# Kernel tuning notes

Hardware: AMD Instinct MI355X
Metric: run time of the kernel (lower is better)

Reference implementation:

```python
import jax, jax.numpy as jnp
import numpy as np

B, C, HD, H, W = 4, 64, 64, 64, 64  # batch, input_dim, hidden_dim, spatial


def conv1x1(x, w, b):
    # x: [B, Cin, H, W], w: [Cout, Cin], b: [Cout]
    return jnp.einsum('oc,bchw->bohw', w, x) + b[None, :, None, None]


def setup_inputs() -> dict:
    key = jax.random.key(0)
    ks = jax.random.split(key, 16)
    sc = lambda cin: 1.0 / np.sqrt(cin)
    d = {
        'h': jax.random.normal(ks[0], (B, C, H, W), jnp.float32),
        'm': jax.random.normal(ks[1], (B, C, H, W), jnp.float32),
        'Wq': jax.random.normal(ks[2], (HD, C), jnp.float32) * sc(C),
        'bq': jnp.zeros((HD,), jnp.float32),
        'Wk': jax.random.normal(ks[3], (HD, C), jnp.float32) * sc(C),
        'bk': jnp.zeros((HD,), jnp.float32),
        'Wk2': jax.random.normal(ks[4], (HD, C), jnp.float32) * sc(C),
        'bk2': jnp.zeros((HD,), jnp.float32),
        'Wv': jax.random.normal(ks[5], (C, C), jnp.float32) * sc(C),
        'bv': jnp.zeros((C,), jnp.float32),
        'Wv2': jax.random.normal(ks[6], (C, C), jnp.float32) * sc(C),
        'bv2': jnp.zeros((C,), jnp.float32),
        'Wz': jax.random.normal(ks[7], (2 * C, 2 * C), jnp.float32) * sc(2 * C),
        'bz': jnp.zeros((2 * C,), jnp.float32),
        'Wm': jax.random.normal(ks[8], (3 * C, 3 * C), jnp.float32) * sc(3 * C),
        'bm': jnp.zeros((3 * C,), jnp.float32),
    }
    return d


def reference(h, m, Wq, bq, Wk, bk, Wk2, bk2, Wv, bv, Wv2, bv2, Wz, bz, Wm, bm):
    b, c, hh, ww = h.shape
    n = hh * ww
    K_h = conv1x1(h, Wk, bk).reshape(b, HD, n)            # [B, HD, N]
    Q_h = conv1x1(h, Wq, bq).reshape(b, HD, n).transpose(0, 2, 1)  # [B, N, HD]
    V_h = conv1x1(h, Wv, bv).reshape(b, c, n)             # [B, C, N]
    K_m = conv1x1(m, Wk2, bk2).reshape(b, HD, n)
    V_m = conv1x1(m, Wv2, bv2).reshape(b, c, n)

    A_h = jax.nn.softmax(jnp.einsum('bnd,bdk->bnk', Q_h, K_h), axis=-1)  # [B, N, N]
    Z_h = jnp.einsum('bnk,bck->bcn', A_h, V_h).reshape(b, c, hh, ww)
    A_m = jax.nn.softmax(jnp.einsum('bnd,bdk->bnk', Q_h, K_m), axis=-1)
    Z_m = jnp.einsum('bnk,bck->bcn', A_m, V_m).reshape(b, c, hh, ww)

    Z = conv1x1(jnp.concatenate([Z_h, Z_m], axis=1), Wz, bz)   # [B, 2C, H, W]
    combined = conv1x1(jnp.concatenate([Z, h], axis=1), Wm, bm)  # [B, 3C, H, W]
    mo, mg, mi = jnp.split(combined, 3, axis=1)
    mi = jax.nn.sigmoid(mi)
    new_m = (1.0 - mi) * m + mi * jnp.tanh(mg)
    new_h = jax.nn.sigmoid(mo) * new_m
    return (new_h, new_m)
```

## Files before the change

### kernel.cpp

```cpp
#include <hip/hip_runtime.h>

#define BN 4
#define NN 4096
#define SPLITK 2
#define LOG2E 1.44269504f
#define MFIX 36.0f

typedef __attribute__((ext_vector_type(8))) __bf16 bf16x8;
typedef __attribute__((ext_vector_type(4))) short s16x4;
typedef __attribute__((ext_vector_type(4))) float f32x4;
typedef unsigned short u16;

__device__ __forceinline__ u16 f2bf(float x) {
  unsigned int u = __builtin_bit_cast(unsigned int, x);
  u = (u + 0x7fffu + ((u >> 16) & 1u)) >> 16;
  return (u16)u;
}
__device__ __forceinline__ u16 f2bfs(float x) {
  __bf16 b = (__bf16)x;
  return __builtin_bit_cast(u16, b);
}
__device__ __forceinline__ float bf2f(u16 s) {
  unsigned int u = ((unsigned int)s) << 16;
  return __builtin_bit_cast(float, u);
}

__device__ __forceinline__ f32x4 mfma16(s16x4 a, s16x4 b, f32x4 c) {
#if defined(__HIP_DEVICE_COMPILE__)
  return __builtin_amdgcn_mfma_f32_16x16x16bf16_1k(a, b, c, 0, 0, 0);
#else
  return c;
#endif
}

__device__ __forceinline__ void gld16(const u16* g, u16* l) {
#if defined(__HIP_DEVICE_COMPILE__)
  __builtin_amdgcn_global_load_lds(
      (const __attribute__((address_space(1))) void*)g,
      (__attribute__((address_space(3))) void*)l, 16, 0, 0);
#else
  (void)g; (void)l;
#endif
}

#define PACK16(A, P0, P1)                                                          \
    P0.x = (unsigned)f2bf(A[0]) | ((unsigned)f2bf(A[1]) << 16);                    \
    P0.y = (unsigned)f2bf(A[2]) | ((unsigned)f2bf(A[3]) << 16);                    \
    P0.z = (unsigned)f2bf(A[4]) | ((unsigned)f2bf(A[5]) << 16);                    \
    P0.w = (unsigned)f2bf(A[6]) | ((unsigned)f2bf(A[7]) << 16);                    \
    P1.x = (unsigned)f2bf(A[8]) | ((unsigned)f2bf(A[9]) << 16);                    \
    P1.y = (unsigned)f2bf(A[10]) | ((unsigned)f2bf(A[11]) << 16);                  \
    P1.z = (unsigned)f2bf(A[12]) | ((unsigned)f2bf(A[13]) << 16);                  \
    P1.w = (unsigned)f2bf(A[14]) | ((unsigned)f2bf(A[15]) << 16);

__global__ void fuse_w_kernel(const float* __restrict__ Wz, const float* __restrict__ bz,
                              const float* __restrict__ Wm, const float* __restrict__ bm,
                              u16* __restrict__ Wbig, float* __restrict__ bbig) {
  int idx = blockIdx.x * 256 + threadIdx.x;
  if (idx < 192 * 192) {
    int o = idx / 192, c = idx - o * 192;
    float v;
    if (c < 128) {
      float s = 0.f;
      for (int j = 0; j < 128; ++j) s = fmaf(Wm[o * 192 + j], Wz[j * 128 + c], s);
      v = s;
    } else {
      v = Wm[o * 192 + c];
    }
    Wbig[idx] = f2bf(v);
  }
  if (idx < 192) {
    float s = bm[idx];
    for (int j = 0; j < 128; ++j) s = fmaf(Wm[idx * 192 + j], bz[j], s);
    bbig[idx] = s;
  }
}

__global__ __launch_bounds__(256) void proj2_kernel(
    const float* __restrict__ h, const float* __restrict__ m,
    const float* __restrict__ Wq, const float* __restrict__ bq,
    const float* __restrict__ Wk, const float* __restrict__ bk,
    const float* __restrict__ Wk2, const float* __restrict__ bk2,
    const float* __restrict__ Wv, const float* __restrict__ bv,
    const float* __restrict__ Wv2, const float* __restrict__ bv2,
    u16* __restrict__ Q, u16* __restrict__ Kh, u16* __restrict__ Km,
    u16* __restrict__ Vh, u16* __restrict__ Vm, u16* __restrict__ hT) {
  __shared__ float xs[64][65];
  int blk = blockIdx.x;
  int ntile = blk & 63, b = (blk >> 6) & 3, pid = blk >> 8;
  int n0 = ntile * 64;
  int t = threadIdx.x, nl = t & 63;
  const float* src = (pid == 2 || pid == 4) ? m : h;
  {
    int c0 = (t >> 6) * 16;
#pragma unroll
    for (int i = 0; i < 16; ++i) {
      int c = c0 + i;
      xs[c][nl] = src[((size_t)(b * 64) + c) * NN + n0 + nl];
    }
  }
  __syncthreads();
  int w = __builtin_amdgcn_readfirstlane(t >> 6);
  size_t nrow = (size_t)b * NN + n0 + nl;
  float acc[16];
  if (pid == 5) {
#pragma unroll
    for (int i = 0; i < 16; ++i) acc[i] = xs[w * 16 + i][nl];
  } else {
    const float* W = pid == 0 ? Wq : pid == 1 ? Wk : pid == 2 ? Wk2 : pid == 3 ? Wv : Wv2;
    const float* bs = pid == 0 ? bq : pid == 1 ? bk : pid == 2 ? bk2 : pid == 3 ? bv : bv2;
#pragma unroll
    for (int i = 0; i < 16; ++i) acc[i] = bs[w * 16 + i];
    for (int c = 0; c < 64; ++c) {
      float x = xs[c][nl];
#pragma unroll
      for (int i = 0; i < 16; ++i) acc[i] = fmaf(W[(w * 16 + i) * 64 + c], x, acc[i]);
    }
    if (pid == 0) {
#pragma unroll
      for (int i = 0; i < 16; ++i) acc[i] *= LOG2E;
    }
  }
  if (pid == 3 || pid == 4) {
    u16* dst = (pid == 3) ? Vh : Vm;
#pragma unroll
    for (int i = 0; i < 16; ++i) {
      int o = w * 16 + i;
      dst[((size_t)(b * 64) + o) * NN + n0 + nl] = f2bf(acc[i]);
    }
  } else {
    u16* dst = pid == 0 ? Q : pid == 1 ? Kh : pid == 2 ? Km : hT;
    uint4 p0, p1;
    PACK16(acc, p0, p1);
    uint4* dp = (uint4*)(dst + nrow * 64 + w * 16);
    dp[0] = p0; dp[1] = p1;
  }
}

__global__ __launch_bounds__(256) void flash6_kernel(
    const u16* __restrict__ Qg, const u16* __restrict__ Khg,
    const u16* __restrict__ Kmg, const u16* __restrict__ Vhg,
    const u16* __restrict__ Vmg, u16* __restrict__ Opart,
    float* __restrict__ Lpart) {
  __shared__ u16 Kl[2][4096];
  __shared__ u16 Vl[2][4096];
  int blk = blockIdx.x;
  int qt = blk & 63, attn = (blk >> 6) & 1, b = (blk >> 7) & 3, split = blk >> 9;
  const u16* K = (attn ? Kmg : Khg) + (size_t)b * NN * 64;
  const u16* V = (attn ? Vmg : Vhg) + (size_t)b * 64 * NN;
  int t = threadIdx.x, wave = t >> 6, lane = t & 63, col = lane & 15, quad = lane >> 4;
  int row0 = qt * 64 + wave * 16;

  const u16* qp = Qg + (size_t)b * NN * 64 + (size_t)(row0 + col) * 64 + quad * 8;
  bf16x8 bq0 = *(const bf16x8*)(const void*)qp;
  bf16x8 bq1 = *(const bf16x8*)(const void*)(qp + 32);

  f32x4 O[4];
#pragma unroll
  for (int i = 0; i < 4; ++i) O[i] = f32x4{0.f, 0.f, 0.f, 0.f};
  f32x4 lacc = {0.f, 0.f, 0.f, 0.f};
  int sp8 = split * 8 + b * 2 + attn;

  const int kbase = split * (NN / SPLITK);
  const int TILES = NN / SPLITK / 64;

#define STAGE(BUF, K0)                                                           \
  _Pragma("unroll") for (int jj = 0; jj < 2; ++jj) {                             \
    int p = jj * 256 + t;                                 \
    int row_ = p >> 3;                                                           \
    int jc_ = (p & 7) ^ (row_ & 7);          \
    gld16(K + (size_t)((K0) + row_) * 64 + jc_ * 8, &Kl[BUF][p * 8]);            \
    gld16(V + (size_t)row_ * NN + (K0) + jc_ * 8, &Vl[BUF][p * 8]);              \
  }

  STAGE(0, kbase);

  for (int kt = 0; kt < TILES; ++kt) {
    __syncthreads();
    int cur = kt & 1;
    if (kt + 1 < TILES) { STAGE(cur ^ 1, kbase + (kt + 1) * 64); }
    const u16* Kb = &Kl[cur][0];
    const u16* Vb = &Vl[cur][0];
    f32x4 St[4];
#pragma unroll
    for (int nt = 0; nt < 4; ++nt) {
      int row = nt * 16 + col;
      int ph0 = row * 8 + (quad ^ (col & 7));
      int ph1 = row * 8 + ((4 + quad) ^ (col & 7));
      bf16x8 a0 = *(const bf16x8*)(const void*)(Kb + ph0 * 8);
      bf16x8 a1 = *(const bf16x8*)(const void*)(Kb + ph1 * 8);
      f32x4 acc = {0.f, 0.f, 0.f, 0.f};
      acc = __builtin_amdgcn_mfma_f32_16x16x32_bf16(a0, bq0, acc, 0, 0, 0);
      acc = __builtin_amdgcn_mfma_f32_16x16x32_bf16(a1, bq1, acc, 0, 0, 0);
      St[nt] = acc;
    }
    s16x4 pfrag[4];
#pragma unroll
    for (int nt = 0; nt < 4; ++nt) {
      f32x4 p;
#pragma unroll
      for (int r = 0; r < 4; ++r) p[r] = __builtin_exp2f(St[nt][r] - MFIX);
      lacc += p;
      s16x4 pf;
#pragma unroll
      for (int r = 0; r < 4; ++r) pf[r] = (short)f2bfs(p[r]);
      pfrag[nt] = pf;
    }
#pragma unroll
    for (int nt = 0; nt < 4; ++nt) {
      int j = nt * 2 + (quad >> 1);
#pragma unroll
      for (int ct = 0; ct < 4; ++ct) {
        int c = ct * 16 + col;
        int ph = c * 8 + (j ^ (col & 7));
        s16x4 vf = *(const s16x4*)(const void*)(Vb + ph * 8 + (quad & 1) * 4);
        O[ct] = mfma16(pfrag[nt], vf, O[ct]);
      }
    }
  }
#undef STAGE

#pragma unroll
  for (int ct = 0; ct < 4; ++ct)
#pragma unroll
    for (int r = 0; r < 4; ++r) {
      size_t q = (size_t)row0 + quad * 4 + r;
      Opart[((size_t)sp8 * NN + q) * 64 + ct * 16 + col] = f2bfs(O[ct][r]);
    }
  float lsum = (lacc[0] + lacc[1]) + (lacc[2] + lacc[3]);
  lsum += __shfl_xor(lsum, 16);
  lsum += __shfl_xor(lsum, 32);
  if (lane < 16) Lpart[(size_t)sp8 * NN + row0 + lane] = lsum;
}

__global__ __launch_bounds__(256) void merge_kernel(
    const u16* __restrict__ Opart, const float* __restrict__ Lpart,
    u16* __restrict__ Zh, u16* __restrict__ Zm) {
  int g = blockIdx.x * 256 + threadIdx.x;
  int c = g & 63;
  int q = (g >> 6) & (NN - 1);
  int b2 = g >> 18;
  size_t i0 = (size_t)b2 * NN + q;
  size_t i1 = (size_t)(8 + b2) * NN + q;
  float L = Lpart[i0] + Lpart[i1];
  float o = bf2f(Opart[i0 * 64 + c]) + bf2f(Opart[i1 * 64 + c]);
  float z = o / L;
  u16* Z = (b2 & 1) ? Zm : Zh;
  int b = b2 >> 1;
  Z[((size_t)b * NN + q) * 64 + c] = f2bfs(z);
}

__global__ __launch_bounds__(256) void epi2_kernel(
    const u16* __restrict__ Wb, const float* __restrict__ bb,
    const u16* __restrict__ Zh, const u16* __restrict__ Zm,
    const u16* __restrict__ hT, const float* __restrict__ mglob,
    float* __restrict__ out) {
  int blk = blockIdx.x;
  int ng = blk * 16;
  int b = ng >> 12;
  int t = threadIdx.x, wave = t >> 6, lane = t & 63, col = lane & 15, quad = lane >> 4;
  size_t nrow = ((size_t)ng + col) * 64;
  bf16x8 bfr[6];
  bfr[0] = *(const bf16x8*)(const void*)(Zh + nrow + quad * 8);
  bfr[1] = *(const bf16x8*)(const void*)(Zh + nrow + 32 + quad * 8);
  bfr[2] = *(const bf16x8*)(const void*)(Zm + nrow + quad * 8);
  bfr[3] = *(const bf16x8*)(const void*)(Zm + nrow + 32 + quad * 8);
  bfr[4] = *(const bf16x8*)(const void*)(hT + nrow + quad * 8);
  bfr[5] = *(const bf16x8*)(const void*)(hT + nrow + 32 + quad * 8);
  f32x4 acc[3];
#pragma unroll
  for (int j = 0; j < 3; ++j) {
    int mt = wave + j * 4;
#pragma unroll
    for (int r = 0; r < 4; ++r) acc[j][r] = bb[mt * 16 + quad * 4 + r];
  }
#pragma unroll
  for (int ks = 0; ks < 6; ++ks) {
#pragma unroll
    for (int j = 0; j < 3; ++j) {
      int mt = wave + j * 4;
      bf16x8 af = *(const bf16x8*)(const void*)(Wb + (size_t)(mt * 16 + col) * 192 + ks * 32 + quad * 8);
      acc[j] = __builtin_amdgcn_mfma_f32_16x16x32_bf16(af, bfr[ks], acc[j], 0, 0, 0);
    }
  }
  int nloc = (ng & (NN - 1)) + col;
#pragma unroll
  for (int r = 0; r < 4; ++r) {
    int o = wave * 16 + quad * 4 + r;
    float mo = acc[0][r], mgt = acc[1][r], mi = acc[2][r];
    float si = 1.f / (1.f + __builtin_exp2f(-mi * LOG2E));
    float tg = 1.f - 2.f / (__builtin_exp2f(2.f * LOG2E * mgt) + 1.f);
    float mv = mglob[(size_t)(b * 64 + o) * NN + nloc];
    float nm = (1.f - si) * mv + si * tg;
    float nh = nm / (1.f + __builtin_exp2f(-mo * LOG2E));
    out[(size_t)(b * 64 + o) * NN + nloc] = nh;
    out[(size_t)BN * 64 * NN + (size_t)(b * 64 + o) * NN + nloc] = nm;
  }
}

extern "C" void kernel_launch(void* const* d_in, const int* in_sizes, int n_in,
                              void* d_out, int out_size, void* d_ws, size_t ws_size,
                              hipStream_t stream) {
  const float* h = (const float*)d_in[0];
  const float* m = (const float*)d_in[1];
  const float* Wq = (const float*)d_in[2];
  const float* bq = (const float*)d_in[3];
  const float* Wk = (const float*)d_in[4];
  const float* bk = (const float*)d_in[5];
  const float* Wk2 = (const float*)d_in[6];
  const float* bk2 = (const float*)d_in[7];
  const float* Wv = (const float*)d_in[8];
  const float* bv = (const float*)d_in[9];
  const float* Wv2 = (const float*)d_in[10];
  const float* bv2 = (const float*)d_in[11];
  const float* Wz = (const float*)d_in[12];
  const float* bz = (const float*)d_in[13];
  const float* Wm = (const float*)d_in[14];
  const float* bm = (const float*)d_in[15];
  float* out = (float*)d_out;

  size_t off = 0;
  auto alloc = [&](size_t bytes) {
    void* p = (char*)d_ws + off;
    off += (bytes + 255) & ~(size_t)255;
    return p;
  };
  const size_t bn64 = (size_t)BN * NN * 64;
  u16* Q  = (u16*)alloc(bn64 * 2);
  u16* Kh = (u16*)alloc(bn64 * 2);
  u16* Km = (u16*)alloc(bn64 * 2);
  u16* Vh = (u16*)alloc(bn64 * 2);
  u16* Vm = (u16*)alloc(bn64 * 2);
  u16* hT = (u16*)alloc(bn64 * 2);
  u16* Zh = (u16*)alloc(bn64 * 2);
  u16* Zm = (u16*)alloc(bn64 * 2);
  u16* Opart = (u16*)alloc((size_t)SPLITK * 8 * NN * 64 * 2);
  float* Lpart = (float*)alloc((size_t)SPLITK * 8 * NN * 4);
  u16* Wbigbf = (u16*)alloc(192 * 192 * 2);
  float* bbig = (float*)alloc(192 * 4);
  (void)ws_size; (void)in_sizes; (void)n_in; (void)out_size;

  fuse_w_kernel<<<144, 256, 0, stream>>>(Wz, bz, Wm, bm, Wbigbf, bbig);
  proj2_kernel<<<6 * BN * 64, 256, 0, stream>>>(h, m, Wq, bq, Wk, bk, Wk2, bk2, Wv, bv,
                                                Wv2, bv2, Q, Kh, Km, Vh, Vm, hT);
  flash6_kernel<<<SPLITK * BN * 2 * 64, 256, 0, stream>>>(Q, Kh, Km, Vh, Vm, Opart, Lpart);
  merge_kernel<<<(BN * 2 * NN * 64) / 256, 256, 0, stream>>>(Opart, Lpart, Zh, Zm);
  epi2_kernel<<<(BN * NN) / 16, 256, 0, stream>>>(Wbigbf, bbig, Zh, Zm, hT, m, out);
}
```

Measured before the change: 206.6 us.

## Fuse split-K merge into epilogue, widen flash blocks to 512 threads

Removes the separate merge kernel. The epilogue now reads both split-K partial outputs and their row sums, normalises them and feeds the result straight into the MFMA projection, which drops the Zh/Zm round trip through global memory. The flash attention kernel moves to 512-thread blocks covering 128 query rows, with a block order that interleaves batch, attention and split, so each staged K/V tile serves twice as many queries. The weight-fusion kernel is rewritten to use one block per output row with the Wm row held in shared memory. The trade-off is fewer, larger attention blocks, which may lower occupancy and latency hiding.

```diff
diff --git a/kernel.cpp b/kernel.cpp
--- a/kernel.cpp
+++ b/kernel.cpp
@@ -53,26 +53,27 @@
     P1.z = (unsigned)f2bf(A[12]) | ((unsigned)f2bf(A[13]) << 16);                  \
     P1.w = (unsigned)f2bf(A[14]) | ((unsigned)f2bf(A[15]) << 16);
 
-__global__ void fuse_w_kernel(const float* __restrict__ Wz, const float* __restrict__ bz,
-                              const float* __restrict__ Wm, const float* __restrict__ bm,
-                              u16* __restrict__ Wbig, float* __restrict__ bbig) {
-  int idx = blockIdx.x * 256 + threadIdx.x;
-  if (idx < 192 * 192) {
-    int o = idx / 192, c = idx - o * 192;
-    float v;
-    if (c < 128) {
-      float s = 0.f;
-      for (int j = 0; j < 128; ++j) s = fmaf(Wm[o * 192 + j], Wz[j * 128 + c], s);
-      v = s;
-    } else {
-      v = Wm[o * 192 + c];
-    }
-    Wbig[idx] = f2bf(v);
-  }
-  if (idx < 192) {
-    float s = bm[idx];
-    for (int j = 0; j < 128; ++j) s = fmaf(Wm[idx * 192 + j], bz[j], s);
-    bbig[idx] = s;
+__global__ __launch_bounds__(256) void fuse_w2_kernel(
+    const float* __restrict__ Wz, const float* __restrict__ bz,
+    const float* __restrict__ Wm, const float* __restrict__ bm,
+    u16* __restrict__ Wbig, float* __restrict__ bbig) {
+  __shared__ float wrow[128];
+  __shared__ float bzs[128];
+  int o = blockIdx.x;
+  int t = threadIdx.x;
+  if (t < 128) { wrow[t] = Wm[o * 192 + t]; bzs[t] = bz[t]; }
+  __syncthreads();
+  if (t < 128) {
+    float s = 0.f;
+#pragma unroll 4
+    for (int j = 0; j < 128; ++j) s = fmaf(wrow[j], Wz[j * 128 + t], s);
+    Wbig[o * 192 + t] = f2bf(s);
+  } else if (t < 192) {
+    Wbig[o * 192 + t] = f2bf(Wm[o * 192 + t]);
+  } else if (t == 192) {
+    float s = bm[o];
+    for (int j = 0; j < 128; ++j) s = fmaf(wrow[j], bzs[j], s);
+    bbig[o] = s;
   }
 }
 
@@ -137,7 +138,7 @@
   }
 }
 
-__global__ __launch_bounds__(256) void flash6_kernel(
+__global__ __launch_bounds__(512) void flash7_kernel(
     const u16* __restrict__ Qg, const u16* __restrict__ Khg,
     const u16* __restrict__ Kmg, const u16* __restrict__ Vhg,
     const u16* __restrict__ Vmg, u16* __restrict__ Opart,
@@ -145,11 +146,12 @@
   __shared__ u16 Kl[2][4096];
   __shared__ u16 Vl[2][4096];
   int blk = blockIdx.x;
-  int qt = blk & 63, attn = (blk >> 6) & 1, b = (blk >> 7) & 3, split = blk >> 9;
+  int combo = blk & 15, qt = blk >> 4;
+  int attn = combo & 1, b = (combo >> 1) & 3, split = combo >> 3;
   const u16* K = (attn ? Kmg : Khg) + (size_t)b * NN * 64;
   const u16* V = (attn ? Vmg : Vhg) + (size_t)b * 64 * NN;
   int t = threadIdx.x, wave = t >> 6, lane = t & 63, col = lane & 15, quad = lane >> 4;
-  int row0 = qt * 64 + wave * 16;
+  int row0 = qt * 128 + wave * 16;
 
   const u16* qp = Qg + (size_t)b * NN * 64 + (size_t)(row0 + col) * 64 + quad * 8;
   bf16x8 bq0 = *(const bf16x8*)(const void*)qp;
@@ -165,8 +167,8 @@
   const int TILES = NN / SPLITK / 64;
 
 #define STAGE(BUF, K0)                                                           \
-  _Pragma("unroll") for (int jj = 0; jj < 2; ++jj) {                             \
-    int p = jj * 256 + t;                                 \
+  {                                                                              \
+    int p = t;                                            \
     int row_ = p >> 3;                                                           \
     int jc_ = (p & 7) ^ (row_ & 7);          \
     gld16(K + (size_t)((K0) + row_) * 64 + jc_ * 8, &Kl[BUF][p * 8]);            \
@@ -233,38 +235,37 @@
   if (lane < 16) Lpart[(size_t)sp8 * NN + row0 + lane] = lsum;
 }
 
-__global__ __launch_bounds__(256) void merge_kernel(
+__global__ __launch_bounds__(256) void epi3_kernel(
+    const u16* __restrict__ Wb, const float* __restrict__ bb,
     const u16* __restrict__ Opart, const float* __restrict__ Lpart,
-    u16* __restrict__ Zh, u16* __restrict__ Zm) {
-  int g = blockIdx.x * 256 + threadIdx.x;
-  int c = g & 63;
-  int q = (g >> 6) & (NN - 1);
-  int b2 = g >> 18;
-  size_t i0 = (size_t)b2 * NN + q;
-  size_t i1 = (size_t)(8 + b2) * NN + q;
-  float L = Lpart[i0] + Lpart[i1];
-  float o = bf2f(Opart[i0 * 64 + c]) + bf2f(Opart[i1 * 64 + c]);
-  float z = o / L;
-  u16* Z = (b2 & 1) ? Zm : Zh;
-  int b = b2 >> 1;
-  Z[((size_t)b * NN + q) * 64 + c] = f2bfs(z);
-}
-
-__global__ __launch_bounds__(256) void epi2_kernel(
-    const u16* __restrict__ Wb, const float* __restrict__ bb,
-    const u16* __restrict__ Zh, const u16* __restrict__ Zm,
     const u16* __restrict__ hT, const float* __restrict__ mglob,
     float* __restrict__ out) {
   int blk = blockIdx.x;
   int ng = blk * 16;
   int b = ng >> 12;
   int t = threadIdx.x, wave = t >> 6, lane = t & 63, col = lane & 15, quad = lane >> 4;
+  int qb = (ng & (NN - 1)) + col;
+  int s0h = b * 2, s1h = 8 + b * 2, s0m = b * 2 + 1, s1m = 9 + b * 2;
+  float invLh = 1.f / (Lpart[(size_t)s0h * NN + qb] + Lpart[(size_t)s1h * NN + qb]);
+  float invLm = 1.f / (Lpart[(size_t)s0m * NN + qb] + Lpart[(size_t)s1m * NN + qb]);
   size_t nrow = ((size_t)ng + col) * 64;
   bf16x8 bfr[6];
-  bfr[0] = *(const bf16x8*)(const void*)(Zh + nrow + quad * 8);
-  bfr[1] = *(const bf16x8*)(const void*)(Zh + nrow + 32 + quad * 8);
-  bfr[2] = *(const bf16x8*)(const void*)(Zm + nrow + quad * 8);
-  bfr[3] = *(const bf16x8*)(const void*)(Zm + nrow + 32 + quad * 8);
+#define MERGEF(DST, SP0, SP1, OFF, INVL)                                         \
+  {                                                                              \
+    const u16* p0_ = Opart + ((size_t)(SP0) * NN + qb) * 64 + (OFF);             \
+    const u16* p1_ = Opart + ((size_t)(SP1) * NN + qb) * 64 + (OFF);             \
+    bf16x8 a_ = *(const bf16x8*)(const void*)p0_;                                \
+    bf16x8 c_ = *(const bf16x8*)(const void*)p1_;                                \
+    bf16x8 r_;                                                                   \
+    _Pragma("unroll") for (int i = 0; i < 8; ++i)                                \
+      r_[i] = (__bf16)(((float)a_[i] + (float)c_[i]) * (INVL));                  \
+    DST = r_;                                                                    \
+  }
+  MERGEF(bfr[0], s0h, s1h, quad * 8, invLh);
+  MERGEF(bfr[1], s0h, s1h, 32 + quad * 8, invLh);
+  MERGEF(bfr[2], s0m, s1m, quad * 8, invLm);
+  MERGEF(bfr[3], s0m, s1m, 32 + quad * 8, invLm);
+#undef MERGEF
   bfr[4] = *(const bf16x8*)(const void*)(hT + nrow + quad * 8);
   bfr[5] = *(const bf16x8*)(const void*)(hT + nrow + 32 + quad * 8);
   f32x4 acc[3];
@@ -332,18 +333,15 @@
   u16* Vh = (u16*)alloc(bn64 * 2);
   u16* Vm = (u16*)alloc(bn64 * 2);
   u16* hT = (u16*)alloc(bn64 * 2);
-  u16* Zh = (u16*)alloc(bn64 * 2);
-  u16* Zm = (u16*)alloc(bn64 * 2);
   u16* Opart = (u16*)alloc((size_t)SPLITK * 8 * NN * 64 * 2);
   float* Lpart = (float*)alloc((size_t)SPLITK * 8 * NN * 4);
   u16* Wbigbf = (u16*)alloc(192 * 192 * 2);
   float* bbig = (float*)alloc(192 * 4);
   (void)ws_size; (void)in_sizes; (void)n_in; (void)out_size;
 
-  fuse_w_kernel<<<144, 256, 0, stream>>>(Wz, bz, Wm, bm, Wbigbf, bbig);
+  fuse_w2_kernel<<<192, 256, 0, stream>>>(Wz, bz, Wm, bm, Wbigbf, bbig);
   proj2_kernel<<<6 * BN * 64, 256, 0, stream>>>(h, m, Wq, bq, Wk, bk, Wk2, bk2, Wv, bv,
                                                 Wv2, bv2, Q, Kh, Km, Vh, Vm, hT);
-  flash6_kernel<<<SPLITK * BN * 2 * 64, 256, 0, stream>>>(Q, Kh, Km, Vh, Vm, Opart, Lpart);
-  merge_kernel<<<(BN * 2 * NN * 64) / 256, 256, 0, stream>>>(Opart, Lpart, Zh, Zm);
-  epi2_kernel<<<(BN * NN) / 16, 256, 0, stream>>>(Wbigbf, bbig, Zh, Zm, hT, m, out);
-}
+  flash7_kernel<<<512, 512, 0, stream>>>(Q, Kh, Km, Vh, Vm, Opart, Lpart);
+  epi3_kernel<<<(BN * NN) / 16, 256, 0, stream>>>(Wbigbf, bbig, Opart, Lpart, hT, m, out);
+}
```

After: 199.5 us. -3.4%, faster.
